# Performance work log

Measured on AMD Instinct MI355X. Metric: run time of the kernel, lower is better.

The kernel has to match this reference:

```python
import jax, jax.numpy as jnp
import numpy as np

HID = 128
OUT = 64
LAYERS = 2
N_ACT, N_RS, N_RD = 100000, 20000, 50000
E_F, E_RS, E_RD, E_HRD = 1600000, 800000, 800000, 800000
NEG_SLOPE = 0.2  # PyG GATConv default


def setup_inputs() -> dict:
    key = jax.random.key(0)
    k = jax.random.split(key, 20)
    s = 1.0 / np.sqrt(HID)
    inp = {
        "x_act": jax.random.normal(k[0], (N_ACT, HID), jnp.float32),
        "x_rs": jax.random.normal(k[1], (N_RS, HID), jnp.float32),
        "x_rd": jax.random.normal(k[2], (N_RD, HID), jnp.float32),
        "ef_src": jax.random.randint(k[3], (E_F,), 0, N_ACT, jnp.int32),
        "ef_dst": jax.random.randint(k[4], (E_F,), 0, N_ACT, jnp.int32),
        "ers_src": jax.random.randint(k[5], (E_RS,), 0, N_ACT, jnp.int32),
        "ers_dst": jax.random.randint(k[6], (E_RS,), 0, N_RS, jnp.int32),
        "erd_src": jax.random.randint(k[7], (E_RD,), 0, N_RD, jnp.int32),
        "erd_dst": jax.random.randint(k[8], (E_RD,), 0, N_RD, jnp.int32),
        "ehrd_src": jax.random.randint(k[9], (E_HRD,), 0, N_ACT, jnp.int32),
        "ehrd_dst": jax.random.randint(k[10], (E_HRD,), 0, N_RD, jnp.int32),
        # GAT params stacked [n_rel=4, layers=2, ...]; rel order: follows, has_rs, rd_delta, has_rd
        "Wsrc": jax.random.normal(k[11], (4, LAYERS, HID, HID), jnp.float32) * s,
        "Wdst": jax.random.normal(k[12], (4, LAYERS, HID, HID), jnp.float32) * s,
        "att_src": jax.random.normal(k[13], (4, LAYERS, HID), jnp.float32) * s,
        "att_dst": jax.random.normal(k[14], (4, LAYERS, HID), jnp.float32) * s,
        "b_gat": jnp.zeros((4, LAYERS, HID), jnp.float32),
        "W_ln": jax.random.normal(k[15], (HID, HID), jnp.float32) * s,
        "b_ln": jnp.zeros((HID,), jnp.float32),
        "W_fc": jax.random.normal(k[16], (HID, OUT), jnp.float32) * s,
        "b_fc": jnp.zeros((OUT,), jnp.float32),
    }
    return inp


def _gat(x_src, x_dst, src, dst, Ws, Wd, a_s, a_d, b):
    """Single-head PyG GATConv (add_self_loops=False), bipartite."""
    n_dst = x_dst.shape[0]
    hs = x_src @ Ws                       # [Nsrc, HID]
    hd = x_dst @ Wd                       # [Ndst, HID]
    e = jax.nn.leaky_relu((hs @ a_s)[src] + (hd @ a_d)[dst], NEG_SLOPE)  # [E]
    m = jax.ops.segment_max(e, dst, num_segments=n_dst)
    m = jnp.where(jnp.isfinite(m), m, 0.0)  # empty segments -> harmless 0
    p = jnp.exp(e - m[dst])
    z = jax.ops.segment_sum(p, dst, num_segments=n_dst)
    w = p / jnp.maximum(z, 1e-16)[dst]    # segment softmax over incoming edges
    out = jax.ops.segment_sum(w[:, None] * hs[src], dst, num_segments=n_dst)
    return out + b


def reference(x_act, x_rs, x_rd, ef_src, ef_dst, ers_src, ers_dst, erd_src, erd_dst,
              ehrd_src, ehrd_dst, Wsrc, Wdst, att_src, att_dst, b_gat,
              W_ln, b_ln, W_fc, b_fc):
    xa, xrs, xrd = x_act, x_rs, x_rd
    for L in range(LAYERS):
        a_new = _gat(xa, xa, ef_src, ef_dst, Wsrc[0, L], Wdst[0, L],
                     att_src[0, L], att_dst[0, L], b_gat[0, L])
        rs_new = _gat(xa, xrs, ers_src, ers_dst, Wsrc[1, L], Wdst[1, L],
                      att_src[1, L], att_dst[1, L], b_gat[1, L])
        # HeteroConv aggr='sum': resource_dynamic gets two conv outputs summed
        rd_new = (_gat(xrd, xrd, erd_src, erd_dst, Wsrc[2, L], Wdst[2, L],
                       att_src[2, L], att_dst[2, L], b_gat[2, L])
                  + _gat(xa, xrd, ehrd_src, ehrd_dst, Wsrc[3, L], Wdst[3, L],
                         att_src[3, L], att_dst[3, L], b_gat[3, L]))
        xa, xrs, xrd = jax.nn.relu(a_new), jax.nn.relu(rs_new), jax.nn.relu(rd_new)
    feats = jnp.stack([jnp.mean(jax.nn.relu(x @ W_ln + b_ln), axis=0)
                       for x in (xa, xrs, xrd)])  # [3, HID]
    pooled = jnp.mean(feats, axis=0)
    return pooled @ W_fc + b_fc  # [OUT]
```

## Files before the change

### kernel.cpp

```cpp
#include <hip/hip_runtime.h>
#include <cmath>

#define HID 128

typedef __attribute__((ext_vector_type(8))) short bf16x8;
typedef __attribute__((ext_vector_type(4))) float f32x4;

__device__ inline unsigned short f2bf_rne(float f) {
  unsigned int b = __float_as_uint(f);
  return (unsigned short)((b + 0x7fffu + ((b >> 16) & 1u)) >> 16);
}
__device__ inline float bf2f(unsigned int u) { return __uint_as_float(u << 16); }

#define NDTOT 220000
#define ETOT 4000000
#define BSH 8
#define BDST 256
#define NB 860
#define EPB 16384
#define NBINBLK 245


__global__ void fill_f_kernel(float* p, float v, int n) {
  int i = blockIdx.x * 256 + threadIdx.x;
  if (i < n) p[i] = v;
}

__global__ void fill_i_kernel(int* p, int v, int n) {
  int i = blockIdx.x * 256 + threadIdx.x;
  if (i < n) p[i] = v;
}

__global__ void f2bf_kernel(const float* __restrict__ in, unsigned short* __restrict__ out,
                            int n8) {
  int i = blockIdx.x * 256 + threadIdx.x;
  if (i >= n8) return;
  const float4* p4 = reinterpret_cast<const float4*>(in) + (size_t)i * 2;
  float4 v0 = p4[0], v1 = p4[1];
  float vv[8] = {v0.x, v0.y, v0.z, v0.w, v1.x, v1.y, v1.z, v1.w};
  unsigned int r[8];
#pragma unroll
  for (int j = 0; j < 8; ++j) r[j] = f2bf_rne(vv[j]);
  uint4 o;
  o.x = r[0] | (r[1] << 16);
  o.y = r[2] | (r[3] << 16);
  o.z = r[4] | (r[5] << 16);
  o.w = r[6] | (r[7] << 16);
  reinterpret_cast<uint4*>(out)[i] = o;
}

__global__ void pack_w_kernel(const float* __restrict__ Wsrc8, const float* __restrict__ W_ln,
                              unsigned short* __restrict__ Wp) {
  int g = blockIdx.y;
  const float* W = (g < 8) ? (Wsrc8 + (size_t)g * 16384) : W_ln;
  unsigned short* op = Wp + (size_t)g * 16384;
  int o = blockIdx.x * 256 + threadIdx.x;
  if (o >= 16384) return;
  int j = o & 7;
  int lane = (o >> 3) & 63;
  int kk = (o >> 9) & 3;
  int ct = (o >> 11) & 3;
  int half = (o >> 13) & 1;
  int k = kk * 32 + ((lane >> 4) * 8) + j;
  int col = half * 64 + ct * 16 + (lane & 15);
  op[o] = f2bf_rne(W[k * 128 + col]);
}

__global__ void compute_v_kernel(const float* __restrict__ W, const float* __restrict__ a,
                                 float* __restrict__ v) {
  int g = blockIdx.x, k = threadIdx.x;
  const float* Wg = W + g * 16384;
  const float* ag = a + g * 128;
  float s = 0.f;
  for (int c = 0; c < 128; ++c) s = fmaf(Wg[k * 128 + c], ag[c], s);
  v[g * 128 + k] = s;
}

template <int NV>
__global__ __launch_bounds__(256) void matvecN_kernel(
    const unsigned short* __restrict__ X, const float* __restrict__ v0,
    const float* __restrict__ v1, const float* __restrict__ v2, const float* __restrict__ v3,
    float* __restrict__ o0, float* __restrict__ o1, float* __restrict__ o2,
    float* __restrict__ o3, int N) {
  __shared__ float vl[NV][128];
  int tid = threadIdx.x;
  if (tid < 128) {
    vl[0][tid] = v0[tid];
    if (NV > 1) vl[1][tid] = v1[tid];
    if (NV > 2) vl[2][tid] = v2[tid];
    if (NV > 3) vl[3][tid] = v3[tid];
  }
  __syncthreads();
  int wave = tid >> 6, lane = tid & 63;
  int row = blockIdx.x * 4 + wave;
  if (row >= N) return;
  unsigned int u = *reinterpret_cast<const unsigned int*>(X + (size_t)row * 128 + lane * 2);
  float x0 = bf2f(u & 0xffffu), x1 = bf2f(u >> 16);
  float a[NV];
#pragma unroll
  for (int j = 0; j < NV; ++j) a[j] = x0 * vl[j][lane * 2] + x1 * vl[j][lane * 2 + 1];
#pragma unroll
  for (int j = 0; j < NV; ++j) {
    float s = a[j];
#pragma unroll
    for (int off = 32; off >= 1; off >>= 1) s += __shfl_down(s, off);
    a[j] = s;
  }
  if (lane == 0) {
    o0[row] = a[0];
    if (NV > 1) o1[row] = a[1];
    if (NV > 2) o2[row] = a[2];
    if (NV > 3) o3[row] = a[3];
  }
}

__global__ void max4_kernel(const float* __restrict__ a0, const float* __restrict__ a1,
                            const float* __restrict__ a2, const float* __restrict__ a3,
                            int n0, int n1, int n2, int n3, unsigned int* __restrict__ outm) {
  int y = blockIdx.y;
  const float* a = (y == 0) ? a0 : (y == 1) ? a1 : (y == 2) ? a2 : a3;
  int n = (y == 0) ? n0 : (y == 1) ? n1 : (y == 2) ? n2 : n3;
  float m = 0.f;
  for (int i = blockIdx.x * 256 + threadIdx.x; i < n; i += gridDim.x * 256)
    m = fmaxf(m, fabsf(a[i]));
#pragma unroll
  for (int off = 32; off >= 1; off >>= 1) m = fmaxf(m, __shfl_xor(m, off));
  if ((threadIdx.x & 63) == 0) atomicMax(&outm[y], __float_as_uint(m));
}


__device__ inline void decode_edge(int e, const int* __restrict__ s0, const int* __restrict__ d0,
                                   const int* __restrict__ s1, const int* __restrict__ d1,
                                   const int* __restrict__ s2, const int* __restrict__ d2,
                                   const int* __restrict__ s3, const int* __restrict__ d3,
                                   int& src, int& gd) {
  const int* sp; const int* dp; int base, doff;
  if (e < 1600000)      { sp = s0; dp = d0; base = 0;       doff = 0; }
  else if (e < 2400000) { sp = s1; dp = d1; base = 1600000; doff = 100000; }
  else if (e < 3200000) { sp = s2; dp = d2; base = 2400000; doff = 120000; }
  else                  { sp = s3; dp = d3; base = 3200000; doff = 170000; }
  int i = e - base;
  src = sp[i];
  gd = doff + dp[i];
}

__global__ __launch_bounds__(256) void bin_hist_kernel(
    const int* __restrict__ d0, const int* __restrict__ d1, const int* __restrict__ d2,
    const int* __restrict__ d3, int* __restrict__ bcnt) {
  __shared__ int lh[NB];
  for (int i = threadIdx.x; i < NB; i += 256) lh[i] = 0;
  __syncthreads();
  int e0 = blockIdx.x * EPB;
  for (int i = 0; i < EPB; i += 256) {
    int e = e0 + i + threadIdx.x;
    if (e < ETOT) {
      const int* dp; int base, doff;
      if (e < 1600000)      { dp = d0; base = 0;       doff = 0; }
      else if (e < 2400000) { dp = d1; base = 1600000; doff = 100000; }
      else if (e < 3200000) { dp = d2; base = 2400000; doff = 120000; }
      else                  { dp = d3; base = 3200000; doff = 170000; }
      atomicAdd(&lh[(doff + dp[e - base]) >> BSH], 1);
    }
  }
  __syncthreads();
  for (int i = threadIdx.x; i < NB; i += 256)
    if (lh[i]) atomicAdd(&bcnt[i], lh[i]);
}

__global__ void scan_nb_kernel(const int* __restrict__ bcnt, int* __restrict__ bbase) {
  if (threadIdx.x == 0 && blockIdx.x == 0) {
    int run = 0;
    for (int b = 0; b < NB; ++b) { bbase[b] = run; run += bcnt[b]; }
    bbase[NB] = run;
  }
}

__global__ __launch_bounds__(256) void bin_scatter_kernel(
    const int* __restrict__ s0, const int* __restrict__ d0, const int* __restrict__ s1,
    const int* __restrict__ d1, const int* __restrict__ s2, const int* __restrict__ d2,
    const int* __restrict__ s3, const int* __restrict__ d3, const int* __restrict__ bbase,
    int* __restrict__ bfill, int2* __restrict__ pair_buf) {
  __shared__ int lh[NB];
  __shared__ int lbase[NB];
  for (int i = threadIdx.x; i < NB; i += 256) lh[i] = 0;
  __syncthreads();
  int e0 = blockIdx.x * EPB;
  for (int i = 0; i < EPB; i += 256) {
    int e = e0 + i + threadIdx.x;
    if (e < ETOT) {
      const int* dp; int base, doff;
      if (e < 1600000)      { dp = d0; base = 0;       doff = 0; }
      else if (e < 2400000) { dp = d1; base = 1600000; doff = 100000; }
      else if (e < 3200000) { dp = d2; base = 2400000; doff = 120000; }
      else                  { dp = d3; base = 3200000; doff = 170000; }
      atomicAdd(&lh[(doff + dp[e - base]) >> BSH], 1);
    }
  }
  __syncthreads();
  for (int i = threadIdx.x; i < NB; i += 256) {
    int c = lh[i];
    if (c) lbase[i] = bbase[i] + atomicAdd(&bfill[i], c);
    lh[i] = 0;
  }
  __syncthreads();
  for (int i = 0; i < EPB; i += 256) {
    int e = e0 + i + threadIdx.x;
    if (e < ETOT) {
      int src, gd;
      decode_edge(e, s0, d0, s1, d1, s2, d2, s3, d3, src, gd);
      int b = gd >> BSH;
      int pos = atomicAdd(&lh[b], 1);
      pair_buf[lbase[b] + pos] = make_int2(src, gd);
    }
  }
}

__global__ __launch_bounds__(256) void bucket_build_kernel(
    const int2* __restrict__ pair_buf, const int* __restrict__ bbase,
    int* __restrict__ rowptr_cat, int* __restrict__ csr_cat) {
  __shared__ int lcnt[BDST];
  __shared__ int lrp[BDST + 1];
  int b = blockIdx.x;
  int d0 = b << BSH;
  int nd = min(BDST, NDTOT - d0);
  int base = bbase[b], end = bbase[b + 1];
  for (int i = threadIdx.x; i < nd; i += 256) lcnt[i] = 0;
  __syncthreads();
  for (int j = base + threadIdx.x; j < end; j += 256)
    atomicAdd(&lcnt[pair_buf[j].y - d0], 1);
  __syncthreads();
  if (threadIdx.x == 0) {
    int run = base;
    for (int i = 0; i < nd; ++i) { lrp[i] = run; run += lcnt[i]; }
    lrp[nd] = run;
  }
  __syncthreads();
  for (int i = threadIdx.x; i <= nd; i += 256) rowptr_cat[d0 + i] = lrp[i];
  for (int i = threadIdx.x; i < nd; i += 256) lcnt[i] = 0;
  __syncthreads();
  for (int j = base + threadIdx.x; j < end; j += 256) {
    int2 pr = pair_buf[j];
    int ld = pr.y - d0;
    int pos = lrp[ld] + atomicAdd(&lcnt[ld], 1);
    csr_cat[pos] = pr.x;
  }
}

__global__ __launch_bounds__(256) void gat_aggr_fused(
    const int* __restrict__ rowptr_cat, const int* __restrict__ csr_cat,
    const float* __restrict__ af_s, const float* __restrict__ af_d,
    const float* __restrict__ ars_s, const float* __restrict__ ars_d,
    const float* __restrict__ ard_s, const float* __restrict__ ard_d,
    const float* __restrict__ ahrd_s, const float* __restrict__ ahrd_d,
    const unsigned int* __restrict__ asmax, const unsigned short* __restrict__ xa,
    const unsigned short* __restrict__ xrd, unsigned short* __restrict__ aggh) {
  __shared__ float2 sp[4][64];
  int wave = threadIdx.x >> 6, lane = threadIdx.x & 63;
  int g = lane >> 4, li = lane & 15;
  int gd = blockIdx.x * 4 + wave;
  if (gd >= NDTOT) return;
  const float* as_; const float* ad_; const unsigned short* Xh; int midx, d;
  if (gd < 100000)      { as_ = af_s;  ad_ = af_d;  Xh = xa;  midx = 0; d = gd; }
  else if (gd < 120000) { as_ = ars_s; ad_ = ars_d; Xh = xa;  midx = 1; d = gd - 100000; }
  else if (gd < 170000) { as_ = ard_s; ad_ = ard_d; Xh = xrd; midx = 3; d = gd - 120000; }
  else                  { as_ = ahrd_s; ad_ = ahrd_d; Xh = xa; midx = 2; d = gd - 170000; }
  int beg = rowptr_cat[gd], end = rowptr_cat[gd + 1];
  float ad = ad_[d];
  float t0 = __uint_as_float(asmax[midx]) + ad;
  float mh = t0 > 0.f ? t0 : 0.2f * t0;
  float z = 0.f;
  float a[8] = {};
  for (int c0 = beg; c0 < end; c0 += 64) {
    int j = c0 + lane;
    int s = 0;
    float p = 0.f;
    if (j < end) {
      s = csr_cat[j];
      float t = as_[s] + ad;
      float e = t > 0.f ? t : 0.2f * t;
      p = __expf(e - mh);
      z += p;
    }
    sp[wave][lane] = make_float2(__int_as_float(s), p);
    asm volatile("s_waitcnt lgkmcnt(0)" ::: "memory");
    int cnt = min(64, end - c0);
    for (int k = 0; k < cnt; k += 4) {
      int idx = k + g;
      if (idx < cnt) {
        float2 w2 = sp[wave][idx];
        int s2 = __float_as_int(w2.x);
        float wgt = w2.y;
        const uint4 xv = *reinterpret_cast<const uint4*>(Xh + (size_t)s2 * 128 + li * 8);
        a[0] = fmaf(wgt, bf2f(xv.x & 0xffffu), a[0]);
        a[1] = fmaf(wgt, bf2f(xv.x >> 16), a[1]);
        a[2] = fmaf(wgt, bf2f(xv.y & 0xffffu), a[2]);
        a[3] = fmaf(wgt, bf2f(xv.y >> 16), a[3]);
        a[4] = fmaf(wgt, bf2f(xv.z & 0xffffu), a[4]);
        a[5] = fmaf(wgt, bf2f(xv.z >> 16), a[5]);
        a[6] = fmaf(wgt, bf2f(xv.w & 0xffffu), a[6]);
        a[7] = fmaf(wgt, bf2f(xv.w >> 16), a[7]);
      }
    }
  }
#pragma unroll
  for (int off = 32; off >= 1; off >>= 1) z += __shfl_xor(z, off);
#pragma unroll
  for (int i = 0; i < 8; ++i) {
    a[i] += __shfl_xor(a[i], 32);
    a[i] += __shfl_xor(a[i], 16);
  }
  if (g == 0) {
    float inv = 1.f / fmaxf(z, 1e-16f);
    uint4 o;
    o.x = (unsigned)f2bf_rne(a[0] * inv) | ((unsigned)f2bf_rne(a[1] * inv) << 16);
    o.y = (unsigned)f2bf_rne(a[2] * inv) | ((unsigned)f2bf_rne(a[3] * inv) << 16);
    o.z = (unsigned)f2bf_rne(a[4] * inv) | ((unsigned)f2bf_rne(a[5] * inv) << 16);
    o.w = (unsigned)f2bf_rne(a[6] * inv) | ((unsigned)f2bf_rne(a[7] * inv) << 16);
    *reinterpret_cast<uint4*>(aggh + (size_t)gd * 128 + li * 8) = o;
  }
}

__global__ __launch_bounds__(256) void gemm_mfma_kernel(
    const unsigned short* __restrict__ X, const unsigned short* __restrict__ Wp,
    const float* __restrict__ bias, unsigned short* __restrict__ Yh, int N) {
  int wid = threadIdx.x >> 6, lane = threadIdx.x & 63;
  int half = blockIdx.y;
  int r0 = blockIdx.x * 128 + wid * 32;
  int lr = lane & 15, gk = lane >> 4;
  bf16x8 b[4][4];
#pragma unroll
  for (int ct = 0; ct < 4; ++ct)
#pragma unroll
    for (int kk = 0; kk < 4; ++kk)
      b[ct][kk] = *reinterpret_cast<const bf16x8*>(Wp + ((((half * 4 + ct) * 4 + kk) * 64 + lane) << 3));
  f32x4 acc[2][4];
#pragma unroll
  for (int rt = 0; rt < 2; ++rt)
#pragma unroll
    for (int ct = 0; ct < 4; ++ct) acc[rt][ct] = (f32x4){0.f, 0.f, 0.f, 0.f};
  int row0 = r0 + lr, row1 = r0 + 16 + lr;
#pragma unroll
  for (int kk = 0; kk < 4; ++kk) {
    bf16x8 a0 = {}, a1 = {};
    if (row0 < N) a0 = *reinterpret_cast<const bf16x8*>(X + (size_t)row0 * 128 + kk * 32 + gk * 8);
    if (row1 < N) a1 = *reinterpret_cast<const bf16x8*>(X + (size_t)row1 * 128 + kk * 32 + gk * 8);
#pragma unroll
    for (int ct = 0; ct < 4; ++ct) {
      acc[0][ct] = __builtin_amdgcn_mfma_f32_16x16x32_bf16(a0, b[ct][kk], acc[0][ct], 0, 0, 0);
      acc[1][ct] = __builtin_amdgcn_mfma_f32_16x16x32_bf16(a1, b[ct][kk], acc[1][ct], 0, 0, 0);
    }
  }
#pragma unroll
  for (int rt = 0; rt < 2; ++rt)
#pragma unroll
    for (int ct = 0; ct < 4; ++ct) {
      int col = half * 64 + ct * 16 + lr;
      float bcol = bias[col];
#pragma unroll
      for (int reg = 0; reg < 4; ++reg) {
        int row = r0 + rt * 16 + gk * 4 + reg;
        if (row < N) {
          float o = acc[rt][ct][reg] + bcol;
          Yh[(size_t)row * 128 + col] = f2bf_rne(fmaxf(o, 0.f));
        }
      }
    }
}

__global__ __launch_bounds__(256) void gemm_mfma2_kernel(
    const unsigned short* __restrict__ X1, const unsigned short* __restrict__ X2,
    const unsigned short* __restrict__ Wp1, const unsigned short* __restrict__ Wp2,
    const float* __restrict__ b1, const float* __restrict__ b2,
    unsigned short* __restrict__ Yh, int N) {
  int wid = threadIdx.x >> 6, lane = threadIdx.x & 63;
  int half = blockIdx.y;
  int r0 = blockIdx.x * 128 + wid * 32;
  int lr = lane & 15, gk = lane >> 4;
  f32x4 acc[2][4];
#pragma unroll
  for (int rt = 0; rt < 2; ++rt)
#pragma unroll
    for (int ct = 0; ct < 4; ++ct) acc[rt][ct] = (f32x4){0.f, 0.f, 0.f, 0.f};
  int row0 = r0 + lr, row1 = r0 + 16 + lr;
  for (int ph = 0; ph < 2; ++ph) {
    const unsigned short* X = ph ? X2 : X1;
    const unsigned short* Wp = ph ? Wp2 : Wp1;
    bf16x8 b[4][4];
#pragma unroll
    for (int ct = 0; ct < 4; ++ct)
#pragma unroll
      for (int kk = 0; kk < 4; ++kk)
        b[ct][kk] = *reinterpret_cast<const bf16x8*>(Wp + ((((half * 4 + ct) * 4 + kk) * 64 + lane) << 3));
#pragma unroll
    for (int kk = 0; kk < 4; ++kk) {
      bf16x8 a0 = {}, a1 = {};
      if (row0 < N) a0 = *reinterpret_cast<const bf16x8*>(X + (size_t)row0 * 128 + kk * 32 + gk * 8);
      if (row1 < N) a1 = *reinterpret_cast<const bf16x8*>(X + (size_t)row1 * 128 + kk * 32 + gk * 8);
#pragma unroll
      for (int ct = 0; ct < 4; ++ct) {
        acc[0][ct] = __builtin_amdgcn_mfma_f32_16x16x32_bf16(a0, b[ct][kk], acc[0][ct], 0, 0, 0);
        acc[1][ct] = __builtin_amdgcn_mfma_f32_16x16x32_bf16(a1, b[ct][kk], acc[1][ct], 0, 0, 0);
      }
    }
  }
#pragma unroll
  for (int rt = 0; rt < 2; ++rt)
#pragma unroll
    for (int ct = 0; ct < 4; ++ct) {
      int col = half * 64 + ct * 16 + lr;
      float bcol = b1[col] + b2[col];
#pragma unroll
      for (int reg = 0; reg < 4; ++reg) {
        int row = r0 + rt * 16 + gk * 4 + reg;
        if (row < N) {
          float o = acc[rt][ct][reg] + bcol;
          Yh[(size_t)row * 128 + col] = f2bf_rne(fmaxf(o, 0.f));
        }
      }
    }
}

__global__ __launch_bounds__(256) void head_fused_kernel(
    const unsigned short* __restrict__ xa, const unsigned short* __restrict__ xrs,
    const unsigned short* __restrict__ xrd, const unsigned short* __restrict__ Wp,
    const float* __restrict__ bias, float* __restrict__ feat) {
  __shared__ float cs[64];
  int bx = blockIdx.x;
  const unsigned short* X; float* f; int N, bx0;
  if (bx < 196)      { X = xa;  f = feat;       N = 100000; bx0 = bx; }
  else if (bx < 236) { X = xrs; f = feat + 128; N = 20000;  bx0 = bx - 196; }
  else               { X = xrd; f = feat + 256; N = 50000;  bx0 = bx - 236; }
  int wid = threadIdx.x >> 6, lane = threadIdx.x & 63;
  int half = blockIdx.y;
  int lr = lane & 15, gk = lane >> 4;
  if (threadIdx.x < 64) cs[threadIdx.x] = 0.f;
  __syncthreads();
  bf16x8 b[4][4];
#pragma unroll
  for (int ct = 0; ct < 4; ++ct)
#pragma unroll
    for (int kk = 0; kk < 4; ++kk)
      b[ct][kk] = *reinterpret_cast<const bf16x8*>(Wp + ((((half * 4 + ct) * 4 + kk) * 64 + lane) << 3));
  float colsum[4] = {0.f, 0.f, 0.f, 0.f};
  for (int c = 0; c < 4; ++c) {
    int r0 = bx0 * 512 + c * 128 + wid * 32;
    if (r0 >= N) break;
    f32x4 acc[2][4];
#pragma unroll
    for (int rt = 0; rt < 2; ++rt)
#pragma unroll
      for (int ct = 0; ct < 4; ++ct) acc[rt][ct] = (f32x4){0.f, 0.f, 0.f, 0.f};
    int row0 = r0 + lr, row1 = r0 + 16 + lr;
#pragma unroll
    for (int kk = 0; kk < 4; ++kk) {
      bf16x8 a0 = {}, a1 = {};
      if (row0 < N) a0 = *reinterpret_cast<const bf16x8*>(X + (size_t)row0 * 128 + kk * 32 + gk * 8);
      if (row1 < N) a1 = *reinterpret_cast<const bf16x8*>(X + (size_t)row1 * 128 + kk * 32 + gk * 8);
#pragma unroll
      for (int ct = 0; ct < 4; ++ct) {
        acc[0][ct] = __builtin_amdgcn_mfma_f32_16x16x32_bf16(a0, b[ct][kk], acc[0][ct], 0, 0, 0);
        acc[1][ct] = __builtin_amdgcn_mfma_f32_16x16x32_bf16(a1, b[ct][kk], acc[1][ct], 0, 0, 0);
      }
    }
#pragma unroll
    for (int rt = 0; rt < 2; ++rt)
#pragma unroll
      for (int ct = 0; ct < 4; ++ct) {
        float bcol = bias[half * 64 + ct * 16 + lr];
#pragma unroll
        for (int reg = 0; reg < 4; ++reg) {
          int row = r0 + rt * 16 + gk * 4 + reg;
          if (row < N) colsum[ct] += fmaxf(acc[rt][ct][reg] + bcol, 0.f);
        }
      }
  }
#pragma unroll
  for (int ct = 0; ct < 4; ++ct) {
    float v = colsum[ct];
    v += __shfl_xor(v, 16);
    v += __shfl_xor(v, 32);
    if (gk == 0) atomicAdd(&cs[ct * 16 + lr], v);
  }
  __syncthreads();
  if (threadIdx.x < 64) atomicAdd(&f[half * 64 + threadIdx.x], cs[threadIdx.x]);
}

__global__ void final_fc_kernel(const float* __restrict__ fa, const float* __restrict__ frs,
                                const float* __restrict__ frd, const float* __restrict__ Wfc,
                                const float* __restrict__ bfc, float* __restrict__ out) {
  __shared__ float pooled[128];
  int t = threadIdx.x;
  if (t < 128)
    pooled[t] = (fa[t] * (1.f / 100000.f) + frs[t] * (1.f / 20000.f) + frd[t] * (1.f / 50000.f)) *
                (1.f / 3.f);
  __syncthreads();
  if (t < 64) {
    float s = bfc[t];
    for (int c = 0; c < 128; ++c) s = fmaf(pooled[c], Wfc[c * 64 + t], s);
    out[t] = s;
  }
}


extern "C" void kernel_launch(void* const* d_in, const int* in_sizes, int n_in,
                              void* d_out, int out_size, void* d_ws, size_t ws_size,
                              hipStream_t stream) {
  const int N_ACT = 100000, N_RS = 20000, N_RD = 50000;

  const float* x_act = (const float*)d_in[0];
  const float* x_rs = (const float*)d_in[1];
  const float* x_rd = (const float*)d_in[2];
  const int* ef_src = (const int*)d_in[3];
  const int* ef_dst = (const int*)d_in[4];
  const int* ers_src = (const int*)d_in[5];
  const int* ers_dst = (const int*)d_in[6];
  const int* erd_src = (const int*)d_in[7];
  const int* erd_dst = (const int*)d_in[8];
  const int* ehrd_src = (const int*)d_in[9];
  const int* ehrd_dst = (const int*)d_in[10];
  const float* Wsrc = (const float*)d_in[11];
  const float* Wdst = (const float*)d_in[12];
  const float* att_src = (const float*)d_in[13];
  const float* att_dst = (const float*)d_in[14];
  const float* b_gat = (const float*)d_in[15];
  const float* W_ln = (const float*)d_in[16];
  const float* b_ln = (const float*)d_in[17];
  const float* W_fc = (const float*)d_in[18];
  const float* b_fc = (const float*)d_in[19];
  float* out = (float*)d_out;

  float* w = (float*)d_ws;
  float* af_s = w;   w += N_ACT;
  float* af_d = w;   w += N_ACT;
  float* ars_s = w;  w += N_ACT;
  float* ahrd_s = w; w += N_ACT;
  float* ard_s = w;  w += N_RD;
  float* ard_d = w;  w += N_RD;
  float* ahrd_d = w; w += N_RD;
  float* ars_d = w;  w += N_RS;
  float* vs = w;    w += 1024;
  float* vd = w;    w += 1024;
  float* feats = w; w += 384;
  unsigned int* asmax_u = (unsigned int*)w; w += 16;
  unsigned short* xa0 = (unsigned short*)w;   w += (size_t)N_ACT * 64;
  unsigned short* xa1 = (unsigned short*)w;   w += (size_t)N_ACT * 64;
  unsigned short* xrd0 = (unsigned short*)w;  w += (size_t)N_RD * 64;
  unsigned short* xrd1 = (unsigned short*)w;  w += (size_t)N_RD * 64;
  unsigned short* xrs_b = (unsigned short*)w; w += (size_t)N_RS * 64;
  unsigned short* aggh = (unsigned short*)w;  w += (size_t)NDTOT * 64;
  unsigned short* wpack = (unsigned short*)w; w += (9 * 16384) / 2;
  int* ip = (int*)w;
  int2* pair_buf = (int2*)ip; ip += 2 * ETOT;
  int* csr_cat = ip;          ip += ETOT;
  int* rowptr_cat = ip;       ip += NDTOT + 1;
  int* bcnt = ip;             ip += NB;
  int* bfill = ip;            ip += NB;
  int* bbase = ip;            ip += NB + 1;

  fill_i_kernel<<<(2 * NB + 255) / 256, 256, 0, stream>>>(bcnt, 0, 2 * NB);
  bin_hist_kernel<<<NBINBLK, 256, 0, stream>>>(ef_dst, ers_dst, erd_dst, ehrd_dst, bcnt);
  scan_nb_kernel<<<1, 64, 0, stream>>>(bcnt, bbase);
  bin_scatter_kernel<<<NBINBLK, 256, 0, stream>>>(
      ef_src, ef_dst, ers_src, ers_dst, erd_src, erd_dst, ehrd_src, ehrd_dst,
      bbase, bfill, pair_buf);
  bucket_build_kernel<<<NB, 256, 0, stream>>>(pair_buf, bbase, rowptr_cat, csr_cat);

  compute_v_kernel<<<8, 128, 0, stream>>>(Wsrc, att_src, vs);
  compute_v_kernel<<<8, 128, 0, stream>>>(Wdst, att_dst, vd);
  pack_w_kernel<<<dim3(64, 9), 256, 0, stream>>>(Wsrc, W_ln, wpack);
  f2bf_kernel<<<(N_ACT * 16 + 255) / 256, 256, 0, stream>>>(x_act, xa0, N_ACT * 16);
  f2bf_kernel<<<(N_RS * 16 + 255) / 256, 256, 0, stream>>>(x_rs, xrs_b, N_RS * 16);
  f2bf_kernel<<<(N_RD * 16 + 255) / 256, 256, 0, stream>>>(x_rd, xrd0, N_RD * 16);

  const unsigned short* xa = xa0;
  unsigned short* xa_nxt = xa1;
  const unsigned short* xrd = xrd0;
  unsigned short* xrd_nxt = xrd1;

  for (int L = 0; L < 2; ++L) {
    matvecN_kernel<4><<<(N_ACT + 3) / 4, 256, 0, stream>>>(
        xa, vs + (0 + L) * 128, vd + (0 + L) * 128, vs + (2 + L) * 128, vs + (6 + L) * 128,
        af_s, af_d, ars_s, ahrd_s, N_ACT);
    matvecN_kernel<3><<<(N_RD + 3) / 4, 256, 0, stream>>>(
        xrd, vs + (4 + L) * 128, vd + (4 + L) * 128, vd + (6 + L) * 128, nullptr,
        ard_s, ard_d, ahrd_d, nullptr, N_RD);
    matvecN_kernel<1><<<(N_RS + 3) / 4, 256, 0, stream>>>(
        xrs_b, vd + (2 + L) * 128, nullptr, nullptr, nullptr,
        ars_d, nullptr, nullptr, nullptr, N_RS);

    fill_i_kernel<<<1, 64, 0, stream>>>((int*)asmax_u, 0, 16);
    max4_kernel<<<dim3(32, 4), 256, 0, stream>>>(af_s, ars_s, ahrd_s, ard_s,
                                                 N_ACT, N_ACT, N_ACT, N_RD, asmax_u);

    gat_aggr_fused<<<(NDTOT + 3) / 4, 256, 0, stream>>>(
        rowptr_cat, csr_cat, af_s, af_d, ars_s, ars_d, ard_s, ard_d, ahrd_s, ahrd_d,
        asmax_u, xa, xrd, aggh);

    int g0 = 0 + L, g1 = 2 + L, g2 = 4 + L, g3 = 6 + L;
    gemm_mfma_kernel<<<dim3((N_ACT + 127) / 128, 2), 256, 0, stream>>>(
        aggh, wpack + (size_t)g0 * 16384, b_gat + g0 * 128, xa_nxt, N_ACT);
    gemm_mfma_kernel<<<dim3((N_RS + 127) / 128, 2), 256, 0, stream>>>(
        aggh + (size_t)100000 * 128, wpack + (size_t)g1 * 16384, b_gat + g1 * 128, xrs_b, N_RS);
    gemm_mfma2_kernel<<<dim3((N_RD + 127) / 128, 2), 256, 0, stream>>>(
        aggh + (size_t)120000 * 128, aggh + (size_t)170000 * 128,
        wpack + (size_t)g2 * 16384, wpack + (size_t)g3 * 16384,
        b_gat + g2 * 128, b_gat + g3 * 128, xrd_nxt, N_RD);

    const unsigned short* t1 = xa; xa = xa_nxt; xa_nxt = (unsigned short*)t1;
    const unsigned short* t2 = xrd; xrd = xrd_nxt; xrd_nxt = (unsigned short*)t2;
  }

  fill_f_kernel<<<2, 256, 0, stream>>>(feats, 0.f, 384);
  head_fused_kernel<<<dim3(334, 2), 256, 0, stream>>>(xa, xrs_b, xrd,
                                                      wpack + (size_t)8 * 16384, b_ln, feats);
  final_fc_kernel<<<1, 128, 0, stream>>>(feats, feats + 128, feats + 256, W_fc, b_fc, out);
}
```

Measured before the change: 732.2 us.

## Fuse per-type matvec and GEMM launches; unroll gather loop in GAT aggregation

The three matvecN launches become one kernel covering all 170k rows, with each 16-lane group handling a row and four outputs computed per row. The three GEMM launches become one kernel that selects the node type from the block index. The GAT aggregation inner loop now issues four independent row gathers per iteration instead of one, giving more memory-level parallelism. These changes cut launch count and tail effects, at the cost of branch divergence and extra register pressure from the unrolled loads.

```diff
diff --git a/kernel.cpp b/kernel.cpp
--- a/kernel.cpp
+++ b/kernel.cpp
@@ -76,41 +76,71 @@
   v[g * 128 + k] = s;
 }
 
-template <int NV>
-__global__ __launch_bounds__(256) void matvecN_kernel(
-    const unsigned short* __restrict__ X, const float* __restrict__ v0,
-    const float* __restrict__ v1, const float* __restrict__ v2, const float* __restrict__ v3,
-    float* __restrict__ o0, float* __restrict__ o1, float* __restrict__ o2,
-    float* __restrict__ o3, int N) {
-  __shared__ float vl[NV][128];
+__device__ inline const float* pick_vec(int r, const float* vs, const float* vd, int L) {
+  switch (r) {
+    case 0: return vs + (0 + L) * 128;
+    case 1: return vd + (0 + L) * 128;
+    case 2: return vs + (2 + L) * 128;
+    case 3: return vs + (6 + L) * 128;
+    case 4: return vs + (4 + L) * 128;
+    case 5: return vd + (4 + L) * 128;
+    case 6: return vd + (6 + L) * 128;
+    default: return vd + (2 + L) * 128;
+  }
+}
+
+__global__ __launch_bounds__(256) void matvec_fused_kernel(
+    const unsigned short* __restrict__ xa, const unsigned short* __restrict__ xrd,
+    const unsigned short* __restrict__ xrs, const float* __restrict__ vs,
+    const float* __restrict__ vd, int L, float* __restrict__ af_s, float* __restrict__ af_d,
+    float* __restrict__ ars_s, float* __restrict__ ahrd_s, float* __restrict__ ard_s,
+    float* __restrict__ ard_d, float* __restrict__ ahrd_d, float* __restrict__ ars_d) {
+  __shared__ float vl[11][128];
   int tid = threadIdx.x;
-  if (tid < 128) {
-    vl[0][tid] = v0[tid];
-    if (NV > 1) vl[1][tid] = v1[tid];
-    if (NV > 2) vl[2][tid] = v2[tid];
-    if (NV > 3) vl[3][tid] = v3[tid];
-  }
+  for (int i = tid; i < 1024; i += 256) {
+    int r = i >> 7;
+    vl[r][i & 127] = pick_vec(r, vs, vd, L)[i & 127];
+  }
+  for (int i = tid; i < 384; i += 256) vl[8 + (i >> 7)][i & 127] = 0.f;
   __syncthreads();
   int wave = tid >> 6, lane = tid & 63;
-  int row = blockIdx.x * 4 + wave;
-  if (row >= N) return;
-  unsigned int u = *reinterpret_cast<const unsigned int*>(X + (size_t)row * 128 + lane * 2);
-  float x0 = bf2f(u & 0xffffu), x1 = bf2f(u >> 16);
-  float a[NV];
-#pragma unroll
-  for (int j = 0; j < NV; ++j) a[j] = x0 * vl[j][lane * 2] + x1 * vl[j][lane * 2 + 1];
-#pragma unroll
-  for (int j = 0; j < NV; ++j) {
-    float s = a[j];
-#pragma unroll
-    for (int off = 32; off >= 1; off >>= 1) s += __shfl_down(s, off);
-    a[j] = s;
-  }
-  if (lane == 0) {
-    o0[row] = a[0];
-    if (NV > 1) o1[row] = a[1];
-    if (NV > 2) o2[row] = a[2];
-    if (NV > 3) o3[row] = a[3];
+  int sub = lane >> 4, li = lane & 15;
+  int row = blockIdx.x * 16 + wave * 4 + sub;
+  if (row >= 170000) return;
+  const unsigned short* X; int lrow, vbase;
+  if (row < 100000)      { X = xa;  lrow = row;          vbase = 0; }
+  else if (row < 150000) { X = xrd; lrow = row - 100000; vbase = 4; }
+  else                   { X = xrs; lrow = row - 150000; vbase = 7; }
+  const uint4 xv = *reinterpret_cast<const uint4*>(X + (size_t)lrow * 128 + li * 8);
+  float f[8];
+  f[0] = bf2f(xv.x & 0xffffu); f[1] = bf2f(xv.x >> 16);
+  f[2] = bf2f(xv.y & 0xffffu); f[3] = bf2f(xv.y >> 16);
+  f[4] = bf2f(xv.z & 0xffffu); f[5] = bf2f(xv.z >> 16);
+  f[6] = bf2f(xv.w & 0xffffu); f[7] = bf2f(xv.w >> 16);
+  float a0 = 0.f, a1 = 0.f, a2 = 0.f, a3 = 0.f;
+#pragma unroll
+  for (int q = 0; q < 8; ++q) {
+    int col = li * 8 + q;
+    a0 = fmaf(f[q], vl[vbase][col], a0);
+    a1 = fmaf(f[q], vl[vbase + 1][col], a1);
+    a2 = fmaf(f[q], vl[vbase + 2][col], a2);
+    a3 = fmaf(f[q], vl[vbase + 3][col], a3);
+  }
+#pragma unroll
+  for (int off = 8; off >= 1; off >>= 1) {
+    a0 += __shfl_xor(a0, off);
+    a1 += __shfl_xor(a1, off);
+    a2 += __shfl_xor(a2, off);
+    a3 += __shfl_xor(a3, off);
+  }
+  if (li == 0) {
+    if (row < 100000) {
+      af_s[lrow] = a0; af_d[lrow] = a1; ars_s[lrow] = a2; ahrd_s[lrow] = a3;
+    } else if (row < 150000) {
+      ard_s[lrow] = a0; ard_d[lrow] = a1; ahrd_d[lrow] = a2;
+    } else {
+      ars_d[lrow] = a0;
+    }
   }
 }
 
@@ -245,6 +275,18 @@
     csr_cat[pos] = pr.x;
   }
 }
+
+#define ACC8(xv, wgt)                                   \
+  do {                                                  \
+    a[0] = fmaf(wgt, bf2f((xv).x & 0xffffu), a[0]);     \
+    a[1] = fmaf(wgt, bf2f((xv).x >> 16), a[1]);         \
+    a[2] = fmaf(wgt, bf2f((xv).y & 0xffffu), a[2]);     \
+    a[3] = fmaf(wgt, bf2f((xv).y >> 16), a[3]);         \
+    a[4] = fmaf(wgt, bf2f((xv).z & 0xffffu), a[4]);     \
+    a[5] = fmaf(wgt, bf2f((xv).z >> 16), a[5]);         \
+    a[6] = fmaf(wgt, bf2f((xv).w & 0xffffu), a[6]);     \
+    a[7] = fmaf(wgt, bf2f((xv).w >> 16), a[7]);         \
+  } while (0)
 
 __global__ __launch_bounds__(256) void gat_aggr_fused(
     const int* __restrict__ rowptr_cat, const int* __restrict__ csr_cat,
@@ -284,22 +326,23 @@
     sp[wave][lane] = make_float2(__int_as_float(s), p);
     asm volatile("s_waitcnt lgkmcnt(0)" ::: "memory");
     int cnt = min(64, end - c0);
-    for (int k = 0; k < cnt; k += 4) {
-      int idx = k + g;
-      if (idx < cnt) {
-        float2 w2 = sp[wave][idx];
-        int s2 = __float_as_int(w2.x);
-        float wgt = w2.y;
-        const uint4 xv = *reinterpret_cast<const uint4*>(Xh + (size_t)s2 * 128 + li * 8);
-        a[0] = fmaf(wgt, bf2f(xv.x & 0xffffu), a[0]);
-        a[1] = fmaf(wgt, bf2f(xv.x >> 16), a[1]);
-        a[2] = fmaf(wgt, bf2f(xv.y & 0xffffu), a[2]);
-        a[3] = fmaf(wgt, bf2f(xv.y >> 16), a[3]);
-        a[4] = fmaf(wgt, bf2f(xv.z & 0xffffu), a[4]);
-        a[5] = fmaf(wgt, bf2f(xv.z >> 16), a[5]);
-        a[6] = fmaf(wgt, bf2f(xv.w & 0xffffu), a[6]);
-        a[7] = fmaf(wgt, bf2f(xv.w >> 16), a[7]);
-      }
+    for (int k = g; k < cnt; k += 16) {
+      float2 w0 = sp[wave][k];
+      float2 w1 = (k + 4 < cnt) ? sp[wave][k + 4] : make_float2(0.f, 0.f);
+      float2 w2 = (k + 8 < cnt) ? sp[wave][k + 8] : make_float2(0.f, 0.f);
+      float2 w3 = (k + 12 < cnt) ? sp[wave][k + 12] : make_float2(0.f, 0.f);
+      const uint4 x0 = *reinterpret_cast<const uint4*>(
+          Xh + (size_t)(unsigned)__float_as_int(w0.x) * 128 + li * 8);
+      const uint4 x1 = *reinterpret_cast<const uint4*>(
+          Xh + (size_t)(unsigned)__float_as_int(w1.x) * 128 + li * 8);
+      const uint4 x2 = *reinterpret_cast<const uint4*>(
+          Xh + (size_t)(unsigned)__float_as_int(w2.x) * 128 + li * 8);
+      const uint4 x3 = *reinterpret_cast<const uint4*>(
+          Xh + (size_t)(unsigned)__float_as_int(w3.x) * 128 + li * 8);
+      ACC8(x0, w0.y);
+      ACC8(x1, w1.y);
+      ACC8(x2, w2.y);
+      ACC8(x3, w3.y);
     }
   }
 #pragma unroll
@@ -320,69 +363,44 @@
   }
 }
 
-__global__ __launch_bounds__(256) void gemm_mfma_kernel(
-    const unsigned short* __restrict__ X, const unsigned short* __restrict__ Wp,
-    const float* __restrict__ bias, unsigned short* __restrict__ Yh, int N) {
+__global__ __launch_bounds__(256) void gemm_all_kernel(
+    const unsigned short* __restrict__ aggh, const unsigned short* __restrict__ wpack,
+    const float* __restrict__ b_gat, int L, unsigned short* __restrict__ ya,
+    unsigned short* __restrict__ yrs, unsigned short* __restrict__ yrd) {
+  int bx = blockIdx.x;
+  const unsigned short *X1, *X2 = nullptr, *Wp1, *Wp2 = nullptr;
+  const float *bias1, *bias2 = nullptr;
+  unsigned short* Y;
+  int N, r0;
+  if (bx < 782) {
+    int gg = 0 + L;
+    X1 = aggh; Wp1 = wpack + (size_t)gg * 16384; bias1 = b_gat + gg * 128;
+    Y = ya; N = 100000; r0 = bx * 128;
+  } else if (bx < 939) {
+    int gg = 2 + L;
+    X1 = aggh + (size_t)100000 * 128; Wp1 = wpack + (size_t)gg * 16384;
+    bias1 = b_gat + gg * 128;
+    Y = yrs; N = 20000; r0 = (bx - 782) * 128;
+  } else {
+    int g2 = 4 + L, g3 = 6 + L;
+    X1 = aggh + (size_t)120000 * 128; Wp1 = wpack + (size_t)g2 * 16384;
+    bias1 = b_gat + g2 * 128;
+    X2 = aggh + (size_t)170000 * 128; Wp2 = wpack + (size_t)g3 * 16384;
+    bias2 = b_gat + g3 * 128;
+    Y = yrd; N = 50000; r0 = (bx - 939) * 128;
+  }
   int wid = threadIdx.x >> 6, lane = threadIdx.x & 63;
   int half = blockIdx.y;
-  int r0 = blockIdx.x * 128 + wid * 32;
-  int lr = lane & 15, gk = lane >> 4;
-  bf16x8 b[4][4];
-#pragma unroll
-  for (int ct = 0; ct < 4; ++ct)
-#pragma unroll
-    for (int kk = 0; kk < 4; ++kk)
-      b[ct][kk] = *reinterpret_cast<const bf16x8*>(Wp + ((((half * 4 + ct) * 4 + kk) * 64 + lane) << 3));
-  f32x4 acc[2][4];
-#pragma unroll
-  for (int rt = 0; rt < 2; ++rt)
-#pragma unroll
-    for (int ct = 0; ct < 4; ++ct) acc[rt][ct] = (f32x4){0.f, 0.f, 0.f, 0.f};
-  int row0 = r0 + lr, row1 = r0 + 16 + lr;
-#pragma unroll
-  for (int kk = 0; kk < 4; ++kk) {
-    bf16x8 a0 = {}, a1 = {};
-    if (row0 < N) a0 = *reinterpret_cast<const bf16x8*>(X + (size_t)row0 * 128 + kk * 32 + gk * 8);
-    if (row1 < N) a1 = *reinterpret_cast<const bf16x8*>(X + (size_t)row1 * 128 + kk * 32 + gk * 8);
-#pragma unroll
-    for (int ct = 0; ct < 4; ++ct) {
-      acc[0][ct] = __builtin_amdgcn_mfma_f32_16x16x32_bf16(a0, b[ct][kk], acc[0][ct], 0, 0, 0);
-      acc[1][ct] = __builtin_amdgcn_mfma_f32_16x16x32_bf16(a1, b[ct][kk], acc[1][ct], 0, 0, 0);
-    }
-  }
-#pragma unroll
-  for (int rt = 0; rt < 2; ++rt)
-#pragma unroll
-    for (int ct = 0; ct < 4; ++ct) {
-      int col = half * 64 + ct * 16 + lr;
-      float bcol = bias[col];
-#pragma unroll
-      for (int reg = 0; reg < 4; ++reg) {
-        int row = r0 + rt * 16 + gk * 4 + reg;
-        if (row < N) {
-          float o = acc[rt][ct][reg] + bcol;
-          Yh[(size_t)row * 128 + col] = f2bf_rne(fmaxf(o, 0.f));
-        }
-      }
-    }
-}
-
-__global__ __launch_bounds__(256) void gemm_mfma2_kernel(
-    const unsigned short* __restrict__ X1, const unsigned short* __restrict__ X2,
-    const unsigned short* __restrict__ Wp1, const unsigned short* __restrict__ Wp2,
-    const float* __restrict__ b1, const float* __restrict__ b2,
-    unsigned short* __restrict__ Yh, int N) {
-  int wid = threadIdx.x >> 6, lane = threadIdx.x & 63;
-  int half = blockIdx.y;
-  int r0 = blockIdx.x * 128 + wid * 32;
+  int rr0 = r0 + wid * 32;
   int lr = lane & 15, gk = lane >> 4;
   f32x4 acc[2][4];
 #pragma unroll
   for (int rt = 0; rt < 2; ++rt)
 #pragma unroll
     for (int ct = 0; ct < 4; ++ct) acc[rt][ct] = (f32x4){0.f, 0.f, 0.f, 0.f};
-  int row0 = r0 + lr, row1 = r0 + 16 + lr;
-  for (int ph = 0; ph < 2; ++ph) {
+  int row0 = rr0 + lr, row1 = rr0 + 16 + lr;
+  int nph = X2 ? 2 : 1;
+  for (int ph = 0; ph < nph; ++ph) {
     const unsigned short* X = ph ? X2 : X1;
     const unsigned short* Wp = ph ? Wp2 : Wp1;
     bf16x8 b[4][4];
@@ -408,13 +426,13 @@
 #pragma unroll
     for (int ct = 0; ct < 4; ++ct) {
       int col = half * 64 + ct * 16 + lr;
-      float bcol = b1[col] + b2[col];
+      float bcol = bias1[col] + (bias2 ? bias2[col] : 0.f);
 #pragma unroll
       for (int reg = 0; reg < 4; ++reg) {
-        int row = r0 + rt * 16 + gk * 4 + reg;
+        int row = rr0 + rt * 16 + gk * 4 + reg;
         if (row < N) {
           float o = acc[rt][ct][reg] + bcol;
-          Yh[(size_t)row * 128 + col] = f2bf_rne(fmaxf(o, 0.f));
+          Y[(size_t)row * 128 + col] = f2bf_rne(fmaxf(o, 0.f));
         }
       }
     }
@@ -578,15 +596,8 @@
   unsigned short* xrd_nxt = xrd1;
 
   for (int L = 0; L < 2; ++L) {
-    matvecN_kernel<4><<<(N_ACT + 3) / 4, 256, 0, stream>>>(
-        xa, vs + (0 + L) * 128, vd + (0 + L) * 128, vs + (2 + L) * 128, vs + (6 + L) * 128,
-        af_s, af_d, ars_s, ahrd_s, N_ACT);
-    matvecN_kernel<3><<<(N_RD + 3) / 4, 256, 0, stream>>>(
-        xrd, vs + (4 + L) * 128, vd + (4 + L) * 128, vd + (6 + L) * 128, nullptr,
-        ard_s, ard_d, ahrd_d, nullptr, N_RD);
-    matvecN_kernel<1><<<(N_RS + 3) / 4, 256, 0, stream>>>(
-        xrs_b, vd + (2 + L) * 128, nullptr, nullptr, nullptr,
-        ars_d, nullptr, nullptr, nullptr, N_RS);
+    matvec_fused_kernel<<<(170000 + 15) / 16, 256, 0, stream>>>(
+        xa, xrd, xrs_b, vs, vd, L, af_s, af_d, ars_s, ahrd_s, ard_s, ard_d, ahrd_d, ars_d);
 
     fill_i_kernel<<<1, 64, 0, stream>>>((int*)asmax_u, 0, 16);
     max4_kernel<<<dim3(32, 4), 256, 0, stream>>>(af_s, ars_s, ahrd_s, ard_s,
@@ -596,15 +607,8 @@
         rowptr_cat, csr_cat, af_s, af_d, ars_s, ars_d, ard_s, ard_d, ahrd_s, ahrd_d,
         asmax_u, xa, xrd, aggh);
 
-    int g0 = 0 + L, g1 = 2 + L, g2 = 4 + L, g3 = 6 + L;
-    gemm_mfma_kernel<<<dim3((N_ACT + 127) / 128, 2), 256, 0, stream>>>(
-        aggh, wpack + (size_t)g0 * 16384, b_gat + g0 * 128, xa_nxt, N_ACT);
-    gemm_mfma_kernel<<<dim3((N_RS + 127) / 128, 2), 256, 0, stream>>>(
-        aggh + (size_t)100000 * 128, wpack + (size_t)g1 * 16384, b_gat + g1 * 128, xrs_b, N_RS);
-    gemm_mfma2_kernel<<<dim3((N_RD + 127) / 128, 2), 256, 0, stream>>>(
-        aggh + (size_t)120000 * 128, aggh + (size_t)170000 * 128,
-        wpack + (size_t)g2 * 16384, wpack + (size_t)g3 * 16384,
-        b_gat + g2 * 128, b_gat + g3 * 128, xrd_nxt, N_RD);
+    gemm_all_kernel<<<dim3(1330, 2), 256, 0, stream>>>(aggh, wpack, b_gat, L,
+                                                       xa_nxt, xrs_b, xrd_nxt);
 
     const unsigned short* t1 = xa; xa = xa_nxt; xa_nxt = (unsigned short*)t1;
     const unsigned short* t2 = xrd; xrd = xrd_nxt; xrd_nxt = (unsigned short*)t2;
```

After: 624.9 us. -14.7%, faster.
